# Kernel optimization log

Measured on AMD Instinct MI355X. Metric: run time of the kernel, lower is better.

Reference implementation:

```python
import jax, jax.numpy as jnp
import numpy as np

DIM = 768
HEADS = 12
DIM_HEAD = 64
INNER = HEADS * DIM_HEAD  # 768
SCALE = DIM_HEAD ** -0.5
LN_EPS = 1e-5


def setup_inputs() -> dict:
    key = jax.random.key(0)
    ks = jax.random.split(key, 6)
    B, N = 2, 1024
    x = jax.random.normal(ks[0], (B, N, DIM), dtype=jnp.float32)
    ln_g = jnp.ones((DIM,), jnp.float32)
    ln_b = jnp.zeros((DIM,), jnp.float32)
    # torch nn.Linear weights are [out, in]
    w_qkv = jax.random.normal(ks[1], (3 * INNER, DIM), jnp.float32) * (DIM ** -0.5)
    w_out = jax.random.normal(ks[2], (DIM, INNER), jnp.float32) * (INNER ** -0.5)
    b_out = jnp.zeros((DIM,), jnp.float32)
    theta = jax.random.normal(ks[3], (HEADS, HEADS), jnp.float32)
    # xavier_uniform for 12x12
    lim = float(np.sqrt(6.0 / (HEADS + HEADS)))
    gnn_w = jax.random.uniform(ks[4], (HEADS, HEADS), jnp.float32, -lim, lim)
    return {"x": x, "ln_g": ln_g, "ln_b": ln_b, "w_qkv": w_qkv,
            "w_out": w_out, "b_out": b_out, "theta": theta, "gnn_w": gnn_w}


def _dc_crd(attn, theta, gnn_w):
    # attn: [B, H, N, N] treated as image with H=12 channels
    B, H, N, _ = attn.shape
    w = attn.mean(axis=(-2, -1))  # adaptive_avg_pool2d -> [B, H]
    diff = w[:, :, None] - w[:, None, :]  # [B, H, H]
    # abs(1 - exp(-d)/(1+exp(-d))) - 1 == abs(1 - sigmoid(-d)) - 1
    T_w = jnp.abs(1.0 - jax.nn.sigmoid(-diff)) - 1.0
    adj = (T_w + jnp.swapaxes(T_w, -1, -2)) * 0.5 * theta  # [B, H, H]
    attn_flat = attn.reshape(B, H, N * N)
    support = jnp.einsum('ij,bjm->bim', gnn_w, attn_flat)  # W @ features
    out = jax.nn.relu(jnp.einsum('bij,bjm->bim', adj, support))  # spmm(adj, support)
    return out.reshape(B, H, N, N)


def reference(x, ln_g, ln_b, w_qkv, w_out, b_out, theta, gnn_w):
    B, N, D = x.shape
    mu = x.mean(-1, keepdims=True)
    var = x.var(-1, keepdims=True)
    xn = (x - mu) * jax.lax.rsqrt(var + LN_EPS) * ln_g + ln_b
    qkv = xn @ w_qkv.T  # [B, N, 3*INNER]
    q, k, v = jnp.split(qkv, 3, axis=-1)
    def heads(t):
        return t.reshape(B, N, HEADS, DIM_HEAD).transpose(0, 2, 1, 3)
    q, k, v = heads(q), heads(k), heads(v)  # [B, H, N, d]
    dots = jnp.einsum('bhnd,bhmd->bhnm', q, k) * SCALE
    attn = jax.nn.softmax(dots, axis=-1)
    H = _dc_crd(attn, theta, gnn_w)
    out = jnp.einsum('bhnm,bhmd->bhnd', attn + H, v)
    out = out.transpose(0, 2, 1, 3).reshape(B, N, INNER)
    return out @ w_out.T + b_out
```

## Files before the change

### kernel.cpp

```cpp
#include <hip/hip_runtime.h>
#include <hip/hip_bf16.h>
#include <stdint.h>

#define NB 2
#define SEQ 1024
#define DMODEL 768
#define NH 12
#define DH 64
#define SCALE 0.125f
#define LOG2E 1.44269504088896f
#define NCH 4

#define AJ_RS 1288
#define CT_HS 648

typedef __hip_bfloat16 bf16;
typedef __attribute__((ext_vector_type(8))) short short8;
typedef __attribute__((ext_vector_type(4))) short short4v;
typedef __attribute__((ext_vector_type(2))) short s2v;
typedef __attribute__((ext_vector_type(4))) float f32x4;
typedef unsigned long long u64;

__device__ __forceinline__ bf16 f2b(float x){ return __float2bfloat16(x); }
__device__ __forceinline__ short f2bs(float x){
  bf16 h = __float2bfloat16(x); return *reinterpret_cast<short*>(&h);
}
__device__ __forceinline__ float s2f(short u){
  return __uint_as_float(((unsigned)(unsigned short)u) << 16);
}

__device__ __forceinline__ void gl_lds16(const bf16* g, bf16* l){
  __builtin_amdgcn_global_load_lds(
      (const __attribute__((address_space(1))) void*)g,
      (__attribute__((address_space(3))) void*)l, 16, 0, 0);
}

__global__ __launch_bounds__(256) void prep_all(const float* __restrict__ x,
                                                const float* __restrict__ g,
                                                const float* __restrict__ bta,
                                                const float* __restrict__ w1, int n1,
                                                const float* __restrict__ w2, int n2,
                                                const float* __restrict__ theta,
                                                const float* __restrict__ gnn,
                                                bf16* __restrict__ xn,
                                                bf16* __restrict__ wb,
                                                bf16* __restrict__ Mb,
                                                float* __restrict__ l){
  int bx = blockIdx.x, t = threadIdx.x;
  if (bx < 2048){
    const float* xr = x + (size_t)bx*DMODEL;
    float v0[3]; float s = 0.f, s2 = 0.f;
    #pragma unroll
    for (int i=0;i<3;i++){ float val = xr[t+256*i]; v0[i]=val; s+=val; s2+=val*val; }
    __shared__ float sb[256], s2b[256];
    sb[t]=s; s2b[t]=s2; __syncthreads();
    for (int off=128; off>0; off>>=1){
      if (t<off){ sb[t]+=sb[t+off]; s2b[t]+=s2b[t+off]; }
      __syncthreads();
    }
    float mean = sb[0]*(1.f/DMODEL);
    float var  = s2b[0]*(1.f/DMODEL) - mean*mean;
    float rstd = rsqrtf(var + 1e-5f);
    #pragma unroll
    for (int i=0;i<3;i++){
      int c = t+256*i;
      xn[(size_t)bx*DMODEL + c] = f2b((v0[i]-mean)*rstd*g[c] + bta[c]);
    }
  } else if (bx < 2048+2304){
    int i = ((bx-2048)*256 + t)*4;
    const float* src = (i < n1) ? (w1 + i) : (w2 + (i - n1));
    float4 v = *(const float4*)src;
    short4v o = { f2bs(v.x), f2bs(v.y), f2bs(v.z), f2bs(v.w) };
    *(short4v*)&wb[i] = o;
  } else {
    int sub = bx - (2048+2304);
    if (sub == 0){
      #pragma unroll
      for (int e=0;e<2;e++){
        int idx = t + 256*e;
        int i = idx >> 5, j = idx & 31;
        float sacc = 0.f;
        if (i < 12 && j < 12)
          for (int jj=0;jj<12;jj++) sacc += (-0.5f)*theta[i*12+jj] * gnn[jj*12+j];
        bf16 hi = f2b(sacc);
        float lo = sacc - __bfloat162float(hi);
        Mb[idx]       = hi;
        Mb[512 + idx] = f2b(lo);
      }
    } else {
      l[(sub-1)*256 + t] = 0.f;
    }
  }
}

__global__ __launch_bounds__(256) void gemm_qkv(const bf16* __restrict__ A,
                                                const bf16* __restrict__ W,
                                                bf16* __restrict__ q,
                                                bf16* __restrict__ k,
                                                bf16* __restrict__ vt){
  __shared__ bf16 As[128*32];
  __shared__ bf16 Bs[64*32];
  int n0 = blockIdx.x*64, m0 = blockIdx.y*128;
  int t = threadIdx.x, w = t>>6, lane = t&63;
  int ln16 = lane&15, q8 = (lane>>4)*8;
  int wm = w>>1, wn = w&1;
  f32x4 acc[4][2] = {};
  int rB = t>>2, koB = (t&3)*8;
  for (int k0=0; k0<768; k0+=32){
    __syncthreads();
    #pragma unroll
    for (int i=0;i<2;i++){
      int cc = t + i*256;
      int r = cc>>2, ko = (cc&3)*8;
      gl_lds16(&A[(size_t)(m0+r)*768 + k0+ko], &As[(size_t)(w*64 + i*256)*8]);
    }
    gl_lds16(&W[(size_t)(n0+rB)*768 + k0+koB], &Bs[(size_t)(w*64)*8]);
    __syncthreads();
    short8 af[4], bfr[2];
    #pragma unroll
    for (int mi=0;mi<4;mi++) af[mi]  = *(const short8*)&As[(wm*64+mi*16+ln16)*32 + q8];
    #pragma unroll
    for (int ni=0;ni<2;ni++) bfr[ni] = *(const short8*)&Bs[(wn*32+ni*16+ln16)*32 + q8];
    #pragma unroll
    for (int mi=0;mi<4;mi++)
      #pragma unroll
      for (int ni=0;ni<2;ni++)
        acc[mi][ni] = __builtin_amdgcn_mfma_f32_16x16x32_bf16(af[mi], bfr[ni], acc[mi][ni], 0, 0, 0);
  }
  int quad4 = (lane>>4)*4;
  #pragma unroll
  for (int mi=0;mi<4;mi++){
    #pragma unroll
    for (int ni=0;ni<2;ni++){
      int cg = n0 + wn*32 + ni*16 + ln16;
      int which = cg/768; int rem = cg - which*768;
      int h = rem>>6, dd = rem&63;
      #pragma unroll
      for (int r=0;r<4;r++){
        int m = m0 + wm*64 + mi*16 + quad4 + r;
        int bb = m>>10, n = m&1023;
        float val = acc[mi][ni][r];
        if (which==0)      q [((size_t)(bb*NH+h)*SEQ + n)*DH + dd] = f2b(val*(SCALE*LOG2E));
        else if (which==1) k [((size_t)(bb*NH+h)*SEQ + n)*DH + dd] = f2b(val);
        else               vt[((size_t)(bb*NH+h)*DH + dd)*SEQ + n] = f2b(val);
      }
    }
  }
}

__global__ __launch_bounds__(768) void attn_sums(const bf16* __restrict__ q,
                                                 const bf16* __restrict__ k,
                                                 float* __restrict__ l,
                                                 u64* __restrict__ pst){
  int rg = blockIdx.x, ch = blockIdx.y, b = blockIdx.z; int r0 = rg*16;
  int t = threadIdx.x; int h = t>>6; int lane = t&63;
  int ln16 = lane&15, quad = lane>>4; int q8 = quad*8, quad4 = quad*4;
  const bf16* qrow = q + ((size_t)(b*NH+h)*SEQ + r0 + ln16)*DH;
  short8 aq0 = *(const short8*)(qrow + q8);
  short8 aq1 = *(const short8*)(qrow + 32 + q8);
  const bf16* kB = k + ((size_t)(b*NH+h)*SEQ)*DH;
  u64* pb = pst + ((((size_t)(b*NCH+ch)*64 + rg)*NH + h)*16)*64 + lane;
  float ls[4] = {0.f,0.f,0.f,0.f};
  #pragma unroll 4
  for (int i=0;i<16;i++){
    int c0 = ch*256 + i*16;
    const bf16* krow = kB + (size_t)(c0 + ln16)*DH;
    short8 bk0 = *(const short8*)(krow + q8);
    short8 bk1 = *(const short8*)(krow + 32 + q8);
    f32x4 a = {0.f,0.f,0.f,0.f};
    a = __builtin_amdgcn_mfma_f32_16x16x32_bf16(aq0, bk0, a, 0, 0, 0);
    a = __builtin_amdgcn_mfma_f32_16x16x32_bf16(aq1, bk1, a, 0, 0, 0);
    float e0 = exp2f(a[0]), e1 = exp2f(a[1]), e2 = exp2f(a[2]), e3 = exp2f(a[3]);
    ls[0]+=e0; ls[1]+=e1; ls[2]+=e2; ls[3]+=e3;
    unsigned p0 = ((unsigned)(unsigned short)f2bs(e1) << 16) | (unsigned)(unsigned short)f2bs(e0);
    unsigned p1 = ((unsigned)(unsigned short)f2bs(e3) << 16) | (unsigned)(unsigned short)f2bs(e2);
    pb[(size_t)i*64] = ((u64)p1 << 32) | (u64)p0;
  }
  #pragma unroll
  for (int msk=1; msk<16; msk<<=1){
    #pragma unroll
    for (int r=0;r<4;r++) ls[r] += __shfl_xor(ls[r], msk);
  }
  if (ln16 == 0){
    #pragma unroll
    for (int r=0;r<4;r++)
      atomicAdd(&l[((size_t)(b*NH+h))*SEQ + r0 + quad4 + r], ls[r]);
  }
}

__global__ __launch_bounds__(768, 6) void attn_main(const bf16* __restrict__ vt,
                                                    const bf16* __restrict__ Mb,
                                                    const float* __restrict__ l,
                                                    const u64* __restrict__ pst,
                                                    bf16* __restrict__ opart){
  __shared__ __align__(16) bf16 attJ[16*AJ_RS];
  __shared__ __align__(16) bf16 combT[12*CT_HS];
  int rg = blockIdx.x, ch = blockIdx.y, b = blockIdx.z; int r0 = rg*16;
  int t = threadIdx.x; int h = t>>6; int lane = t&63;
  int ln16 = lane&15, quad = lane>>4; int q8 = quad*8, quad4 = quad*4;
  const bf16* vB = vt + ((size_t)(b*NH+h)*DH)*SEQ;
  const u64* pb = pst + ((((size_t)(b*NCH+ch)*64 + rg)*NH + h)*16)*64 + lane;

  short8 z8 = (short8){0,0,0,0,0,0,0,0};
  for (int i = t*8; i < 16*AJ_RS; i += 768*8) *(short8*)&attJ[i] = z8;

  short8 mhi = *(const short8*)&Mb[ln16*32 + q8];
  short8 mlo = *(const short8*)&Mb[512 + ln16*32 + q8];

  float inv_l[4];
  #pragma unroll
  for (int r=0;r<4;r++) inv_l[r] = 1.0f / l[((size_t)(b*NH+h))*SEQ + r0 + quad4 + r];

  u64 cur0 = pb[0*64], cur1 = pb[1*64];

  __syncthreads();

  f32x4 oacc[4] = {};
  for (int it=0; it<8; it++){
    int c0 = ch*256 + it*32;
    const bf16* vp = vB + (size_t)ln16*SEQ + c0 + q8;
    short8 vv0 = *(const short8*)(vp);
    short8 vv1 = *(const short8*)(vp + 16*SEQ);
    short8 vv2 = *(const short8*)(vp + 32*SEQ);
    short8 vv3 = *(const short8*)(vp + 48*SEQ);
    int nx = (it+1)&7;
    u64 n0 = pb[(size_t)(nx*2+0)*64], n1 = pb[(size_t)(nx*2+1)*64];
    #pragma unroll
    for (int half=0; half<2; half++){
      int cc = half*16 + ln16;
      u64 cu = half ? cur1 : cur0;
      unsigned p0 = (unsigned)cu, p1 = (unsigned)(cu >> 32);
      attJ[(quad4+0)*AJ_RS + cc*40 + h] = f2b(s2f((short)(p0 & 0xffff))*inv_l[0]);
      attJ[(quad4+1)*AJ_RS + cc*40 + h] = f2b(s2f((short)(p0 >> 16))   *inv_l[1]);
      attJ[(quad4+2)*AJ_RS + cc*40 + h] = f2b(s2f((short)(p1 & 0xffff))*inv_l[2]);
      attJ[(quad4+3)*AJ_RS + cc*40 + h] = f2b(s2f((short)(p1 >> 16))   *inv_l[3]);
    }
    __syncthreads();
    #pragma unroll
    for (int ii=0; ii<2; ii++){
      int n = (h + ii*12)*16 + ln16;
      int base = (n>>5)*AJ_RS + (n&31)*40;
      short8 bfrag = *(const short8*)&attJ[base + q8];
      f32x4 c = {0.f,0.f,0.f,0.f};
      c = __builtin_amdgcn_mfma_f32_16x16x32_bf16(mlo, bfrag, c, 0, 0, 0);
      c = __builtin_amdgcn_mfma_f32_16x16x32_bf16(mhi, bfrag, c, 0, 0, 0);
      s2v id01 = *(const s2v*)&attJ[base + quad4];
      s2v id23 = *(const s2v*)&attJ[base + quad4 + 2];
      float idf[4] = { s2f(id01[0]), s2f(id01[1]), s2f(id23[0]), s2f(id23[1]) };
      int cbase = (n>>5)*40 + (n&31);
      if (quad < 3){
        #pragma unroll
        for (int ri=0; ri<4; ri++)
          combT[(quad4+ri)*CT_HS + cbase] = f2b(idf[ri] + fmaxf(c[ri], 0.f));
      }
    }
    if (h < 8){
      int n = (h + 24)*16 + ln16;
      int base = (n>>5)*AJ_RS + (n&31)*40;
      short8 bfrag = *(const short8*)&attJ[base + q8];
      f32x4 c = {0.f,0.f,0.f,0.f};
      c = __builtin_amdgcn_mfma_f32_16x16x32_bf16(mlo, bfrag, c, 0, 0, 0);
      c = __builtin_amdgcn_mfma_f32_16x16x32_bf16(mhi, bfrag, c, 0, 0, 0);
      s2v id01 = *(const s2v*)&attJ[base + quad4];
      s2v id23 = *(const s2v*)&attJ[base + quad4 + 2];
      float idf[4] = { s2f(id01[0]), s2f(id01[1]), s2f(id23[0]), s2f(id23[1]) };
      int cbase = (n>>5)*40 + (n&31);
      if (quad < 3){
        #pragma unroll
        for (int ri=0; ri<4; ri++)
          combT[(quad4+ri)*CT_HS + cbase] = f2b(idf[ri] + fmaxf(c[ri], 0.f));
      }
    }
    __syncthreads();
    short8 afrag = *(const short8*)&combT[h*CT_HS + ln16*40 + q8];
    oacc[0] = __builtin_amdgcn_mfma_f32_16x16x32_bf16(afrag, vv0, oacc[0], 0, 0, 0);
    oacc[1] = __builtin_amdgcn_mfma_f32_16x16x32_bf16(afrag, vv1, oacc[1], 0, 0, 0);
    oacc[2] = __builtin_amdgcn_mfma_f32_16x16x32_bf16(afrag, vv2, oacc[2], 0, 0, 0);
    oacc[3] = __builtin_amdgcn_mfma_f32_16x16x32_bf16(afrag, vv3, oacc[3], 0, 0, 0);
    cur0 = n0; cur1 = n1;
  }
  bf16* dst = opart + ((size_t)ch*NB*SEQ + (size_t)b*SEQ)*DMODEL;
  #pragma unroll
  for (int ni=0; ni<4; ni++)
    #pragma unroll
    for (int r=0; r<4; r++){
      int n = r0 + quad4 + r;
      dst[(size_t)n*DMODEL + h*DH + ni*16 + ln16] = f2b(oacc[ni][r]);
    }
}

__global__ __launch_bounds__(256) void reduce_kernel(const bf16* __restrict__ opart,
                                                     bf16* __restrict__ aout){
  const size_t TOT = (size_t)NB*SEQ*DMODEL;
  size_t i = ((size_t)blockIdx.x*256 + threadIdx.x)*8;
  float s[8] = {};
  #pragma unroll
  for (int c=0;c<NCH;c++){
    short8 u = *(const short8*)&opart[c*TOT + i];
    #pragma unroll
    for (int e=0;e<8;e++) s[e] += s2f(u[e]);
  }
  short8 o;
  #pragma unroll
  for (int e=0;e<8;e++) o[e] = f2bs(s[e]);
  *(short8*)&aout[i] = o;
}

__global__ __launch_bounds__(256) void gemm_out(const bf16* __restrict__ A,
                                                const bf16* __restrict__ W,
                                                const float* __restrict__ bias,
                                                float* __restrict__ out){
  __shared__ bf16 As[64*32];
  __shared__ bf16 Bs[64*32];
  int n0 = blockIdx.x*64, m0 = blockIdx.y*64;
  int t = threadIdx.x, w = t>>6, lane = t&63;
  int ln16 = lane&15, q8 = (lane>>4)*8;
  int wm = w>>1, wn = w&1;
  f32x4 acc[2][2] = {};
  int r = t>>2, ko = (t&3)*8;
  for (int k0=0; k0<768; k0+=32){
    __syncthreads();
    gl_lds16(&A[(size_t)(m0+r)*768 + k0+ko], &As[(size_t)(w*64)*8]);
    gl_lds16(&W[(size_t)(n0+r)*768 + k0+ko], &Bs[(size_t)(w*64)*8]);
    __syncthreads();
    short8 af[2], bfr[2];
    #pragma unroll
    for (int mi=0;mi<2;mi++) af[mi]  = *(const short8*)&As[(wm*32+mi*16+ln16)*32 + q8];
    #pragma unroll
    for (int ni=0;ni<2;ni++) bfr[ni] = *(const short8*)&Bs[(wn*32+ni*16+ln16)*32 + q8];
    #pragma unroll
    for (int mi=0;mi<2;mi++)
      #pragma unroll
      for (int ni=0;ni<2;ni++)
        acc[mi][ni] = __builtin_amdgcn_mfma_f32_16x16x32_bf16(af[mi], bfr[ni], acc[mi][ni], 0, 0, 0);
  }
  int quad4 = (lane>>4)*4;
  #pragma unroll
  for (int mi=0;mi<2;mi++)
    #pragma unroll
    for (int ni=0;ni<2;ni++){
      int cg = n0 + wn*32 + ni*16 + ln16;
      #pragma unroll
      for (int rr=0;rr<4;rr++){
        int m = m0 + wm*32 + mi*16 + quad4 + rr;
        out[(size_t)m*768 + cg] = acc[mi][ni][rr] + bias[cg];
      }
    }
}

extern "C" void kernel_launch(void* const* d_in, const int* in_sizes, int n_in,
                              void* d_out, int out_size, void* d_ws, size_t ws_size,
                              hipStream_t stream){
  const float* x     = (const float*)d_in[0];
  const float* ln_g  = (const float*)d_in[1];
  const float* ln_b  = (const float*)d_in[2];
  const float* w_qkv = (const float*)d_in[3];
  const float* w_out = (const float*)d_in[4];
  const float* b_out = (const float*)d_in[5];
  const float* theta = (const float*)d_in[6];
  const float* gnn   = (const float*)d_in[7];
  float* out = (float*)d_out;

  char* p = (char*)d_ws;
  bf16* xnb   = (bf16*)p; p += (size_t)2048*768*2;
  bf16* wqkvb = (bf16*)p; p += (size_t)2304*768*2;
  bf16* woutb = (bf16*)p; p += (size_t)768*768*2;
  bf16* qb    = (bf16*)p; p += (size_t)NB*NH*SEQ*DH*2;
  bf16* kb    = (bf16*)p; p += (size_t)NB*NH*SEQ*DH*2;
  bf16* vtb   = (bf16*)p; p += (size_t)NB*NH*SEQ*DH*2;
  bf16* aoutb = (bf16*)p; p += (size_t)2048*768*2;
  bf16* Mbw   = (bf16*)p; p += (size_t)1024*2;
  float* lsum = (float*)p; p += (size_t)NB*NH*SEQ*4;
  bf16* opart = (bf16*)p; p += (size_t)NCH*NB*SEQ*DMODEL*2;
  u64*  pstw  = (u64*)p;

  const int N1 = 2304*768, N2 = 768*768;
  prep_all<<<dim3(2048+2304+97), dim3(256), 0, stream>>>(
      x, ln_g, ln_b, w_qkv, N1, w_out, N2, theta, gnn, xnb, wqkvb, Mbw, lsum);
  gemm_qkv<<<dim3(36, 16), dim3(256), 0, stream>>>(xnb, wqkvb, qb, kb, vtb);
  attn_sums<<<dim3(64, NCH, NB), dim3(768), 0, stream>>>(qb, kb, lsum, pstw);
  attn_main<<<dim3(64, NCH, NB), dim3(768), 0, stream>>>(vtb, Mbw, lsum, pstw, opart);
  reduce_kernel<<<dim3(NB*SEQ*DMODEL/(8*256)), dim3(256), 0, stream>>>(opart, aoutb);
  gemm_out<<<dim3(12, 32), dim3(256), 0, stream>>>(aoutb, woutb, b_out, out);
}
```

Before: 177.4 us.

## Double-buffer attn_main LDS stages, shrink head-mix MFMA to 16x16x16, use wave-shuffle layernorm

The attention kernel now double-buffers the attJ and combT LDS tiles. The head-mixing stage for one chunk runs alongside the attn×V MFMAs of the previous chunk, which drops one barrier per iteration. The head-mixing MFMA shrinks from 16x16x32 with zero padding to 16x16x16, which halves the attJ row stride and the Mb padding. LayerNorm replaces its shared-memory tree reduction with wave shuffles. Together these cut barriers and wasted MFMA work, at the cost of twice the LDS per block, which may lower occupancy, and a more complex prologue and epilogue.

```diff
diff --git a/kernel.cpp b/kernel.cpp
--- a/kernel.cpp
+++ b/kernel.cpp
@@ -11,7 +11,7 @@
 #define LOG2E 1.44269504088896f
 #define NCH 4
 
-#define AJ_RS 1288
+#define AJ_RS 648
 #define CT_HS 648
 
 typedef __hip_bfloat16 bf16;
@@ -52,14 +52,16 @@
     float v0[3]; float s = 0.f, s2 = 0.f;
     #pragma unroll
     for (int i=0;i<3;i++){ float val = xr[t+256*i]; v0[i]=val; s+=val; s2+=val*val; }
-    __shared__ float sb[256], s2b[256];
-    sb[t]=s; s2b[t]=s2; __syncthreads();
-    for (int off=128; off>0; off>>=1){
-      if (t<off){ sb[t]+=sb[t+off]; s2b[t]+=s2b[t+off]; }
-      __syncthreads();
-    }
-    float mean = sb[0]*(1.f/DMODEL);
-    float var  = s2b[0]*(1.f/DMODEL) - mean*mean;
+    #pragma unroll
+    for (int m=1;m<64;m<<=1){ s += __shfl_xor(s,m); s2 += __shfl_xor(s2,m); }
+    __shared__ float pw[4], pw2[4];
+    int wv = t>>6;
+    if ((t&63)==0){ pw[wv]=s; pw2[wv]=s2; }
+    __syncthreads();
+    float fs  = pw[0]+pw[1]+pw[2]+pw[3];
+    float fs2 = pw2[0]+pw2[1]+pw2[2]+pw2[3];
+    float mean = fs*(1.f/DMODEL);
+    float var  = fs2*(1.f/DMODEL) - mean*mean;
     float rstd = rsqrtf(var + 1e-5f);
     #pragma unroll
     for (int i=0;i<3;i++){
@@ -75,17 +77,15 @@
   } else {
     int sub = bx - (2048+2304);
     if (sub == 0){
-      #pragma unroll
-      for (int e=0;e<2;e++){
-        int idx = t + 256*e;
-        int i = idx >> 5, j = idx & 31;
+      if (t < 256){
+        int i = t >> 4, j = t & 15;
         float sacc = 0.f;
         if (i < 12 && j < 12)
           for (int jj=0;jj<12;jj++) sacc += (-0.5f)*theta[i*12+jj] * gnn[jj*12+j];
         bf16 hi = f2b(sacc);
         float lo = sacc - __bfloat162float(hi);
-        Mb[idx]       = hi;
-        Mb[512 + idx] = f2b(lo);
+        Mb[t]       = hi;
+        Mb[256 + t] = f2b(lo);
       }
     } else {
       l[(sub-1)*256 + t] = 0.f;
@@ -193,8 +193,8 @@
                                                     const float* __restrict__ l,
                                                     const u64* __restrict__ pst,
                                                     bf16* __restrict__ opart){
-  __shared__ __align__(16) bf16 attJ[16*AJ_RS];
-  __shared__ __align__(16) bf16 combT[12*CT_HS];
+  __shared__ __align__(16) bf16 attJ[2][16*AJ_RS];
+  __shared__ __align__(16) bf16 combT[2][12*CT_HS];
   int rg = blockIdx.x, ch = blockIdx.y, b = blockIdx.z; int r0 = rg*16;
   int t = threadIdx.x; int h = t>>6; int lane = t&63;
   int ln16 = lane&15, quad = lane>>4; int q8 = quad*8, quad4 = quad*4;
@@ -202,82 +202,96 @@
   const u64* pb = pst + ((((size_t)(b*NCH+ch)*64 + rg)*NH + h)*16)*64 + lane;
 
   short8 z8 = (short8){0,0,0,0,0,0,0,0};
-  for (int i = t*8; i < 16*AJ_RS; i += 768*8) *(short8*)&attJ[i] = z8;
-
-  short8 mhi = *(const short8*)&Mb[ln16*32 + q8];
-  short8 mlo = *(const short8*)&Mb[512 + ln16*32 + q8];
+  bf16* aj = (bf16*)attJ;
+  for (int i = t*8; i < 2*16*AJ_RS; i += 768*8) *(short8*)&aj[i] = z8;
+
+  short4v mhi4 = *(const short4v*)&Mb[ln16*16 + quad*4];
+  short4v mlo4 = *(const short4v*)&Mb[256 + ln16*16 + quad*4];
 
   float inv_l[4];
   #pragma unroll
   for (int r=0;r<4;r++) inv_l[r] = 1.0f / l[((size_t)(b*NH+h))*SEQ + r0 + quad4 + r];
 
-  u64 cur0 = pb[0*64], cur1 = pb[1*64];
-
-  __syncthreads();
-
-  f32x4 oacc[4] = {};
-  for (int it=0; it<8; it++){
-    int c0 = ch*256 + it*32;
-    const bf16* vp = vB + (size_t)ln16*SEQ + c0 + q8;
-    short8 vv0 = *(const short8*)(vp);
-    short8 vv1 = *(const short8*)(vp + 16*SEQ);
-    short8 vv2 = *(const short8*)(vp + 32*SEQ);
-    short8 vv3 = *(const short8*)(vp + 48*SEQ);
-    int nx = (it+1)&7;
-    u64 n0 = pb[(size_t)(nx*2+0)*64], n1 = pb[(size_t)(nx*2+1)*64];
+  auto A_phase = [&](int bb, u64 c0q, u64 c1q){
+    bf16* dst = &attJ[bb][0];
     #pragma unroll
     for (int half=0; half<2; half++){
       int cc = half*16 + ln16;
-      u64 cu = half ? cur1 : cur0;
+      u64 cu = half ? c1q : c0q;
       unsigned p0 = (unsigned)cu, p1 = (unsigned)(cu >> 32);
-      attJ[(quad4+0)*AJ_RS + cc*40 + h] = f2b(s2f((short)(p0 & 0xffff))*inv_l[0]);
-      attJ[(quad4+1)*AJ_RS + cc*40 + h] = f2b(s2f((short)(p0 >> 16))   *inv_l[1]);
-      attJ[(quad4+2)*AJ_RS + cc*40 + h] = f2b(s2f((short)(p1 & 0xffff))*inv_l[2]);
-      attJ[(quad4+3)*AJ_RS + cc*40 + h] = f2b(s2f((short)(p1 >> 16))   *inv_l[3]);
-    }
-    __syncthreads();
-    #pragma unroll
-    for (int ii=0; ii<2; ii++){
-      int n = (h + ii*12)*16 + ln16;
-      int base = (n>>5)*AJ_RS + (n&31)*40;
-      short8 bfrag = *(const short8*)&attJ[base + q8];
-      f32x4 c = {0.f,0.f,0.f,0.f};
-      c = __builtin_amdgcn_mfma_f32_16x16x32_bf16(mlo, bfrag, c, 0, 0, 0);
-      c = __builtin_amdgcn_mfma_f32_16x16x32_bf16(mhi, bfrag, c, 0, 0, 0);
-      s2v id01 = *(const s2v*)&attJ[base + quad4];
-      s2v id23 = *(const s2v*)&attJ[base + quad4 + 2];
-      float idf[4] = { s2f(id01[0]), s2f(id01[1]), s2f(id23[0]), s2f(id23[1]) };
-      int cbase = (n>>5)*40 + (n&31);
-      if (quad < 3){
-        #pragma unroll
-        for (int ri=0; ri<4; ri++)
-          combT[(quad4+ri)*CT_HS + cbase] = f2b(idf[ri] + fmaxf(c[ri], 0.f));
+      dst[(quad4+0)*AJ_RS + cc*20 + h] = f2b(s2f((short)(p0 & 0xffff))*inv_l[0]);
+      dst[(quad4+1)*AJ_RS + cc*20 + h] = f2b(s2f((short)(p0 >> 16))   *inv_l[1]);
+      dst[(quad4+2)*AJ_RS + cc*20 + h] = f2b(s2f((short)(p1 & 0xffff))*inv_l[2]);
+      dst[(quad4+3)*AJ_RS + cc*20 + h] = f2b(s2f((short)(p1 >> 16))   *inv_l[3]);
+    }
+  };
+  auto mixTile = [&](const bf16* src, bf16* dstC, int tl){
+    int n = tl*16 + ln16;
+    int base = (n>>5)*AJ_RS + (n&31)*20;
+    short4v bfrag = *(const short4v*)&src[base + quad*4];
+    f32x4 c = {0.f,0.f,0.f,0.f};
+    c = __builtin_amdgcn_mfma_f32_16x16x16bf16_1k(mlo4, bfrag, c, 0, 0, 0);
+    c = __builtin_amdgcn_mfma_f32_16x16x16bf16_1k(mhi4, bfrag, c, 0, 0, 0);
+    s2v id01 = *(const s2v*)&src[base + quad4];
+    s2v id23 = *(const s2v*)&src[base + quad4 + 2];
+    float idf[4] = { s2f(id01[0]), s2f(id01[1]), s2f(id23[0]), s2f(id23[1]) };
+    int cbase = (n>>5)*40 + (n&31);
+    if (quad < 3){
+      #pragma unroll
+      for (int ri=0; ri<4; ri++)
+        dstC[(quad4+ri)*CT_HS + cbase] = f2b(idf[ri] + fmaxf(c[ri], 0.f));
+    }
+  };
+
+  u64 cur0 = pb[0], cur1 = pb[64];
+  __syncthreads();
+  A_phase(0, cur0, cur1);
+  u64 nx0 = pb[2*64], nx1 = pb[3*64];
+
+  f32x4 oacc[4] = {};
+  short8 vv0, vv1, vv2, vv3;
+  for (int it=0; it<8; it++){
+    int bb = it&1;
+    if (it > 0){
+      const bf16* vp = vB + (size_t)ln16*SEQ + ch*256 + (it-1)*32 + q8;
+      vv0 = *(const short8*)(vp);
+      vv1 = *(const short8*)(vp + 16*SEQ);
+      vv2 = *(const short8*)(vp + 32*SEQ);
+      vv3 = *(const short8*)(vp + 48*SEQ);
+    }
+    __syncthreads();
+    mixTile(&attJ[bb][0], &combT[bb][0], h);
+    mixTile(&attJ[bb][0], &combT[bb][0], h + 12);
+    if (h < 8) mixTile(&attJ[bb][0], &combT[bb][0], h + 24);
+    if (it > 0){
+      short8 afrag = *(const short8*)&combT[bb^1][h*CT_HS + ln16*40 + q8];
+      oacc[0] = __builtin_amdgcn_mfma_f32_16x16x32_bf16(afrag, vv0, oacc[0], 0, 0, 0);
+      oacc[1] = __builtin_amdgcn_mfma_f32_16x16x32_bf16(afrag, vv1, oacc[1], 0, 0, 0);
+      oacc[2] = __builtin_amdgcn_mfma_f32_16x16x32_bf16(afrag, vv2, oacc[2], 0, 0, 0);
+      oacc[3] = __builtin_amdgcn_mfma_f32_16x16x32_bf16(afrag, vv3, oacc[3], 0, 0, 0);
+    }
+    if (it < 7){
+      A_phase(bb^1, nx0, nx1);
+      if (it < 6){
+        nx0 = pb[(size_t)((it+2)*2)*64];
+        nx1 = pb[(size_t)((it+2)*2+1)*64];
       }
     }
-    if (h < 8){
-      int n = (h + 24)*16 + ln16;
-      int base = (n>>5)*AJ_RS + (n&31)*40;
-      short8 bfrag = *(const short8*)&attJ[base + q8];
-      f32x4 c = {0.f,0.f,0.f,0.f};
-      c = __builtin_amdgcn_mfma_f32_16x16x32_bf16(mlo, bfrag, c, 0, 0, 0);
-      c = __builtin_amdgcn_mfma_f32_16x16x32_bf16(mhi, bfrag, c, 0, 0, 0);
-      s2v id01 = *(const s2v*)&attJ[base + quad4];
-      s2v id23 = *(const s2v*)&attJ[base + quad4 + 2];
-      float idf[4] = { s2f(id01[0]), s2f(id01[1]), s2f(id23[0]), s2f(id23[1]) };
-      int cbase = (n>>5)*40 + (n&31);
-      if (quad < 3){
-        #pragma unroll
-        for (int ri=0; ri<4; ri++)
-          combT[(quad4+ri)*CT_HS + cbase] = f2b(idf[ri] + fmaxf(c[ri], 0.f));
-      }
-    }
-    __syncthreads();
-    short8 afrag = *(const short8*)&combT[h*CT_HS + ln16*40 + q8];
+  }
+  {
+    const bf16* vp = vB + (size_t)ln16*SEQ + ch*256 + 7*32 + q8;
+    vv0 = *(const short8*)(vp);
+    vv1 = *(const short8*)(vp + 16*SEQ);
+    vv2 = *(const short8*)(vp + 32*SEQ);
+    vv3 = *(const short8*)(vp + 48*SEQ);
+  }
+  __syncthreads();
+  {
+    short8 afrag = *(const short8*)&combT[1][h*CT_HS + ln16*40 + q8];
     oacc[0] = __builtin_amdgcn_mfma_f32_16x16x32_bf16(afrag, vv0, oacc[0], 0, 0, 0);
     oacc[1] = __builtin_amdgcn_mfma_f32_16x16x32_bf16(afrag, vv1, oacc[1], 0, 0, 0);
     oacc[2] = __builtin_amdgcn_mfma_f32_16x16x32_bf16(afrag, vv2, oacc[2], 0, 0, 0);
     oacc[3] = __builtin_amdgcn_mfma_f32_16x16x32_bf16(afrag, vv3, oacc[3], 0, 0, 0);
-    cur0 = n0; cur1 = n1;
   }
   bf16* dst = opart + ((size_t)ch*NB*SEQ + (size_t)b*SEQ)*DMODEL;
   #pragma unroll
```

Result: no change. 176.4 us, median of 2 (-0.5%).
